# Performance work log

Measured on AMD Instinct MI355X. Metric: run time of the kernel, lower is better.

The kernel has to match this reference:

```python
import jax, jax.numpy as jnp
import numpy as np

N = 50000      # nodes
E = 800000     # edges (before self loops)
G = 64         # graphs in batch
IN = 128       # in_features
HID = 64       # hidden_dim per head
HEADS = 4
NC = 2         # num_classes
SLOPE = 0.2    # PyG GATConv negative_slope default


def setup_inputs() -> dict:
    key = jax.random.key(0)
    ks = jax.random.split(key, 16)
    s = 0.1
    HC = HID * HEADS
    inp = {
        "x": jax.random.normal(ks[0], (N, IN), jnp.float32),
        "edge_index": jax.random.randint(ks[1], (2, E), 0, N, jnp.int64),
        "batch": jnp.sort(jax.random.randint(ks[2], (N,), 0, G, jnp.int64)),
        # GATConv 1: lin weight [H*C, IN], att vecs [H, C], bias [H*C]
        "W1": jax.random.normal(ks[3], (HC, IN), jnp.float32) * s,
        "as1": jax.random.normal(ks[4], (HEADS, HID), jnp.float32) * s,
        "ad1": jax.random.normal(ks[5], (HEADS, HID), jnp.float32) * s,
        "b1": jnp.zeros((HC,), jnp.float32),
        # GATConv 2
        "W2": jax.random.normal(ks[6], (HC, HC), jnp.float32) * s,
        "as2": jax.random.normal(ks[7], (HEADS, HID), jnp.float32) * s,
        "ad2": jax.random.normal(ks[8], (HEADS, HID), jnp.float32) * s,
        "b2": jnp.zeros((HC,), jnp.float32),
        # GATConv 3
        "W3": jax.random.normal(ks[9], (HC, HC), jnp.float32) * s,
        "as3": jax.random.normal(ks[10], (HEADS, HID), jnp.float32) * s,
        "ad3": jax.random.normal(ks[11], (HEADS, HID), jnp.float32) * s,
        "b3": jnp.zeros((HC,), jnp.float32),
        # MLP head
        "fc1_w": jax.random.normal(ks[12], (HID, HC), jnp.float32) * s,
        "fc1_b": jnp.zeros((HID,), jnp.float32),
        "fc2_w": jax.random.normal(ks[13], (NC, HID), jnp.float32) * s,
        "fc2_b": jnp.zeros((NC,), jnp.float32),
    }
    return inp


def gat_conv(x, src, dst, W, a_src, a_dst, b):
    """PyG-style GATConv (concat=True, self loops already in src/dst)."""
    n = x.shape[0]
    h = (x @ W.T).reshape(n, HEADS, HID)            # [N,H,C]
    al_s = jnp.sum(h * a_src[None], axis=-1)        # [N,H]
    al_d = jnp.sum(h * a_dst[None], axis=-1)        # [N,H]
    e = jax.nn.leaky_relu(al_s[src] + al_d[dst], SLOPE)  # [Et,H]
    # segment softmax over edges grouped by destination node
    m = jax.ops.segment_max(e, dst, num_segments=n)      # [N,H]
    ex = jnp.exp(e - m[dst])
    den = jax.ops.segment_sum(ex, dst, num_segments=n)
    alpha = ex / (den[dst] + 1e-16)                      # [Et,H]
    out = jax.ops.segment_sum(h[src] * alpha[:, :, None], dst, num_segments=n)
    return out.reshape(n, HEADS * HID) + b


def reference(x, edge_index, batch, W1, as1, ad1, b1, W2, as2, ad2, b2,
              W3, as3, ad3, b3, fc1_w, fc1_b, fc2_w, fc2_b):
    loops = jnp.arange(N, dtype=edge_index.dtype)
    src = jnp.concatenate([edge_index[0], loops])   # add_self_loops=True
    dst = jnp.concatenate([edge_index[1], loops])

    h = jax.nn.relu(gat_conv(x, src, dst, W1, as1, ad1, b1))
    h = jax.nn.relu(gat_conv(h, src, dst, W2, as2, ad2, b2))
    h = gat_conv(h, src, dst, W3, as3, ad3, b3)

    # global_mean_pool over batch vector
    sums = jax.ops.segment_sum(h, batch, num_segments=G)          # [G,H*C]
    cnts = jax.ops.segment_sum(jnp.ones((N,), h.dtype), batch, num_segments=G)
    pooled = sums / jnp.maximum(cnts, 1.0)[:, None]

    z = jax.nn.relu(pooled @ fc1_w.T + fc1_b)
    return z @ fc2_w.T + fc2_b                                    # [G,NC]
```

## Files before the change

kernel.cpp:

```cpp
#include <hip/hip_runtime.h>
#include <hip/hip_bf16.h>

#define N_NODES 50000
#define E_EDGES 800000
#define ET (E_EDGES + N_NODES)
#define G_GRAPHS 64
#define IN_F 128
#define HID 64
#define HEADS 4
#define HC (HID * HEADS)
#define NC 2
#define SLOPE 0.2f
#define L2E 1.4426950408889634f

typedef float f32x4 __attribute__((ext_vector_type(4)));
typedef __bf16 bf16x8 __attribute__((ext_vector_type(8)));
typedef unsigned short us8 __attribute__((ext_vector_type(8)));
typedef unsigned short us4 __attribute__((ext_vector_type(4)));
typedef _Float16 h16x4 __attribute__((ext_vector_type(4)));

#define MFMA16(a, b, c) \
  __builtin_amdgcn_mfma_f32_16x16x32_bf16(__builtin_bit_cast(bf16x8, (a)), \
                                          __builtin_bit_cast(bf16x8, (b)), (c), 0, 0, 0)

__device__ inline unsigned short f2bf_rne(float f) {
  unsigned u = __builtin_bit_cast(unsigned, f);
  u += 0x7fffu + ((u >> 16) & 1u);
  return (unsigned short)(u >> 16);
}
__device__ inline float bf2f(unsigned short h) {
  unsigned u = ((unsigned)h) << 16;
  return __builtin_bit_cast(float, u);
}


__device__ inline void split4(const float* __restrict__ in, unsigned short* __restrict__ hi,
                              unsigned short* __restrict__ lo, int i) {
  float4 v = *(const float4*)&in[i];
  float f[4] = {v.x, v.y, v.z, v.w};
  us4 h, l;
#pragma unroll
  for (int j = 0; j < 4; j++) {
    unsigned short hb = f2bf_rne(f[j]);
    h[j] = hb;
    l[j] = f2bf_rne(f[j] - bf2f(hb));
  }
  *(us4*)&hi[i] = h;
  *(us4*)&lo[i] = l;
}

#define QX (N_NODES * IN_F / 4)
#define QW1 (HC * IN_F / 4)
#define QW2 (HC * HC / 4)
#define QTOT (QX + QW1 + 2 * QW2)

__global__ __launch_bounds__(256) void split_all_kernel(
    const float* __restrict__ x, const float* __restrict__ W1,
    const float* __restrict__ W2, const float* __restrict__ W3,
    unsigned short* __restrict__ xhi,
    unsigned short* __restrict__ w1h, unsigned short* __restrict__ w1l,
    unsigned short* __restrict__ w2h, unsigned short* __restrict__ w2l,
    unsigned short* __restrict__ w3h, unsigned short* __restrict__ w3l) {
  int q = blockIdx.x * 256 + threadIdx.x;
  if (q < QX) {
    int i = q * 4;
    float4 v = *(const float4*)&x[i];
    float f[4] = {v.x, v.y, v.z, v.w};
    us4 h;
#pragma unroll
    for (int j = 0; j < 4; j++) h[j] = f2bf_rne(f[j]);
    *(us4*)&xhi[i] = h;
  } else if (q < QX + QW1) {
    split4(W1, w1h, w1l, (q - QX) * 4);
  } else if (q < QX + QW1 + QW2) {
    split4(W2, w2h, w2l, (q - QX - QW1) * 4);
  } else {
    split4(W3, w3h, w3l, (q - QX - QW1 - QW2) * 4);
  }
}


__global__ void count_kernel(const int* __restrict__ ei, int* __restrict__ cnt) {
  int e = blockIdx.x * blockDim.x + threadIdx.x;
  if (e >= ET) return;
  int dst = (e < E_EDGES) ? ei[E_EDGES + e] : (e - E_EDGES);
  atomicAdd(&cnt[dst], 1);
}

#define SCAN_BLOCKS ((N_NODES + 255) / 256)

__global__ __launch_bounds__(256) void scan1_kernel(const int* __restrict__ cnt,
                                                    int* __restrict__ incl_buf,
                                                    int* __restrict__ partial) {
  __shared__ int ws[4];
  int tid = threadIdx.x, b = blockIdx.x;
  int wave = tid >> 6, lane = tid & 63;
  int i = b * 256 + tid;
  int v = (i < N_NODES) ? cnt[i] : 0;
  int x = v;
#pragma unroll
  for (int off = 1; off < 64; off <<= 1) {
    int t = __shfl_up(x, off, 64);
    if (lane >= off) x += t;
  }
  if (lane == 63) ws[wave] = x;
  __syncthreads();
  if (tid == 0) {
    int s = 0;
#pragma unroll
    for (int w = 0; w < 4; w++) { int t = ws[w]; ws[w] = s; s += t; }
    partial[b] = s;
  }
  __syncthreads();
  if (i < N_NODES) incl_buf[i] = x + ws[wave];
}

__global__ __launch_bounds__(256) void scan2_kernel(int* __restrict__ partial) {
  __shared__ int ws[4];
  int tid = threadIdx.x;
  int wave = tid >> 6, lane = tid & 63;
  int v = (tid < SCAN_BLOCKS) ? partial[tid] : 0;
  int x = v;
#pragma unroll
  for (int off = 1; off < 64; off <<= 1) {
    int t = __shfl_up(x, off, 64);
    if (lane >= off) x += t;
  }
  if (lane == 63) ws[wave] = x;
  __syncthreads();
  if (tid == 0) {
    int s = 0;
#pragma unroll
    for (int w = 0; w < 4; w++) { int t = ws[w]; ws[w] = s; s += t; }
  }
  __syncthreads();
  partial[tid] = x + ws[wave] - v;
}

__global__ __launch_bounds__(256) void scan3_kernel(const int* __restrict__ cnt,
                                                    int* __restrict__ incl_buf,
                                                    const int* __restrict__ partial,
                                                    int* __restrict__ rowptr,
                                                    int* __restrict__ cursor) {
  int tid = threadIdx.x, b = blockIdx.x;
  int i = b * 256 + tid;
  if (i >= N_NODES) return;
  int incl = incl_buf[i] + partial[b];
  rowptr[i + 1] = incl;
  cursor[i] = incl - cnt[i];
  if (i == 0) rowptr[0] = 0;
}

__global__ void scatter_kernel(const int* __restrict__ ei, int* __restrict__ cursor,
                               int* __restrict__ csr_src) {
  int e = blockIdx.x * blockDim.x + threadIdx.x;
  if (e >= ET) return;
  int src, dst;
  if (e < E_EDGES) { src = ei[e]; dst = ei[E_EDGES + e]; }
  else { src = e - E_EDGES; dst = src; }
  int pos = atomicAdd(&cursor[dst], 1);
  csr_src[pos] = src;
}


template <int K>
__global__ __launch_bounds__(256) void mfma_gemm_kernel(
    const unsigned short* __restrict__ A,
    const unsigned short* __restrict__ Whi, const unsigned short* __restrict__ Wlo,
    const float* __restrict__ a_s, const float* __restrict__ a_d,
    _Float16* __restrict__ hbuf16, float* __restrict__ als, float* __restrict__ ald) {
  __shared__ unsigned short As[4 * 64 * 8];
  __shared__ unsigned short Bs[2][4 * 256 * 8];

  int t = threadIdx.x;
  int mt = blockIdx.x;
  int w = t >> 6, lane = t & 63, lr = lane & 15, kg = lane >> 4;
  int srow = t >> 2, skg = t & 3;

  f32x4 acc[4][4];
#pragma unroll
  for (int m = 0; m < 4; m++)
#pragma unroll
    for (int nf = 0; nf < 4; nf++) {
      f32x4 z = {0.f, 0.f, 0.f, 0.f};
      acc[m][nf] = z;
    }

  int agrow = mt * 64 + srow;
  bool avalid = agrow < N_NODES;

  us8 va[2], vb0[2][4], vb1[2][4];
  {
    if (avalid) {
      va[0] = *(const us8*)&A[(size_t)agrow * K + skg * 8];
    } else {
      us8 z = {0, 0, 0, 0, 0, 0, 0, 0};
      va[0] = z;
    }
#pragma unroll
    for (int c = 0; c < 4; c++) {
      int n = srow + 64 * c;
      vb0[0][c] = *(const us8*)&Whi[(size_t)n * K + skg * 8];
      vb1[0][c] = *(const us8*)&Wlo[(size_t)n * K + skg * 8];
    }
  }

#pragma unroll
  for (int k0 = 0; k0 < K; k0 += 32) {
    const int buf = (k0 >> 5) & 1;
    const int nbuf = buf ^ 1;
    __syncthreads();
    *(us8*)&As[(skg * 64 + srow) * 8] = va[buf];
#pragma unroll
    for (int c = 0; c < 4; c++) {
      int n = srow + 64 * c;
      *(us8*)&Bs[0][(skg * 256 + n) * 8] = vb0[buf][c];
      *(us8*)&Bs[1][(skg * 256 + n) * 8] = vb1[buf][c];
    }
    __syncthreads();

    if (k0 + 32 < K) {
      int k1 = k0 + 32;
      if (avalid) {
        va[nbuf] = *(const us8*)&A[(size_t)agrow * K + k1 + skg * 8];
      } else {
        us8 z = {0, 0, 0, 0, 0, 0, 0, 0};
        va[nbuf] = z;
      }
#pragma unroll
      for (int c = 0; c < 4; c++) {
        int n = srow + 64 * c;
        vb0[nbuf][c] = *(const us8*)&Whi[(size_t)n * K + k1 + skg * 8];
        vb1[nbuf][c] = *(const us8*)&Wlo[(size_t)n * K + k1 + skg * 8];
      }
    }

    us8 bh[4], bl[4];
#pragma unroll
    for (int nf = 0; nf < 4; nf++) {
      int n = w * 64 + nf * 16 + lr;
      bh[nf] = *(us8*)&Bs[0][(kg * 256 + n) * 8];
      bl[nf] = *(us8*)&Bs[1][(kg * 256 + n) * 8];
    }
#pragma unroll
    for (int m = 0; m < 4; m++) {
      int row = m * 16 + lr;
      us8 ah = *(us8*)&As[(kg * 64 + row) * 8];
#pragma unroll
      for (int nf = 0; nf < 4; nf++) {
        acc[m][nf] = MFMA16(ah, bh[nf], acc[m][nf]);
        acc[m][nf] = MFMA16(ah, bl[nf], acc[m][nf]);
      }
    }
  }

  int head = w;
  float asv[4], adv[4];
#pragma unroll
  for (int nf = 0; nf < 4; nf++) {
    asv[nf] = a_s[head * HID + nf * 16 + lr];
    adv[nf] = a_d[head * HID + nf * 16 + lr];
  }
#pragma unroll
  for (int m = 0; m < 4; m++) {
#pragma unroll
    for (int r = 0; r < 4; r++) {
      int grow = mt * 64 + m * 16 + kg * 4 + r;
      float ps = 0.f, pd = 0.f;
#pragma unroll
      for (int nf = 0; nf < 4; nf++) {
        float v = acc[m][nf][r];
        ps += v * asv[nf];
        pd += v * adv[nf];
        if (grow < N_NODES)
          hbuf16[(size_t)grow * HC + head * 64 + nf * 16 + lr] = (_Float16)v;
      }
#pragma unroll
      for (int msk = 1; msk < 16; msk <<= 1) {
        ps += __shfl_xor(ps, msk, 64);
        pd += __shfl_xor(pd, msk, 64);
      }
      if (lr == 0 && grow < N_NODES) {
        als[grow * HEADS + head] = ps * L2E;
        ald[grow * HEADS + head] = pd * L2E;
      }
    }
  }
}


template <int MODE>
__global__ __launch_bounds__(256) void agg_kernel(
    const _Float16* __restrict__ hbuf16, const float* __restrict__ alsE,
    const float* __restrict__ aldE, const int* __restrict__ rowptr,
    const int* __restrict__ csr_src, const float* __restrict__ bias,
    unsigned short* __restrict__ ohi, float* __restrict__ pooled,
    const int* __restrict__ batch) {
  int wave = threadIdx.x >> 6;
  int lane = threadIdx.x & 63;
  int v0 = blockIdx.x * 8 + wave * 2;
  int v1 = v0 + 1;
  int head = lane >> 4;
  float ald0 = aldE[(unsigned)v0 * HEADS + head];
  float ald1 = aldE[(unsigned)v1 * HEADS + head];
  int beg0 = rowptr[v0], n0 = rowptr[v0 + 1] - beg0;
  int beg1 = rowptr[v1], n1 = rowptr[v1 + 1] - beg1;
  int n = max(n0, n1);

  float den0 = 0.f, den1 = 0.f;
  f32x4 acc0 = {0.f, 0.f, 0.f, 0.f};
  f32x4 acc1 = {0.f, 0.f, 0.f, 0.f};
  const _Float16* hp = hbuf16 + (lane << 2);
#pragma unroll 2
  for (int i = 0; i < n; i++) {
    int s0 = csr_src[beg0 + min(i, n0 - 1)];
    int s1 = csr_src[beg1 + min(i, n1 - 1)];
    float a0 = alsE[(unsigned)s0 * HEADS + head] + ald0;
    float a1 = alsE[(unsigned)s1 * HEADS + head] + ald1;
    a0 = fmaxf(a0, SLOPE * a0);
    a1 = fmaxf(a1, SLOPE * a1);
    float ex0 = (i < n0) ? __builtin_amdgcn_exp2f(a0) : 0.f;
    float ex1 = (i < n1) ? __builtin_amdgcn_exp2f(a1) : 0.f;
    h16x4 h0 = *(const h16x4*)(hp + ((unsigned)s0 << 8));
    h16x4 h1 = *(const h16x4*)(hp + ((unsigned)s1 << 8));
    den0 += ex0; den1 += ex1;
    acc0[0] += (float)h0[0] * ex0; acc0[1] += (float)h0[1] * ex0;
    acc0[2] += (float)h0[2] * ex0; acc0[3] += (float)h0[3] * ex0;
    acc1[0] += (float)h1[0] * ex1; acc1[1] += (float)h1[1] * ex1;
    acc1[2] += (float)h1[2] * ex1; acc1[3] += (float)h1[3] * ex1;
  }
  float inv0 = 1.0f / (den0 + 1e-16f);
  float inv1 = 1.0f / (den1 + 1e-16f);
  float4 bv = *(const float4*)&bias[lane * 4];
  float o0[4], o1[4];
  o0[0] = acc0[0] * inv0 + bv.x; o0[1] = acc0[1] * inv0 + bv.y;
  o0[2] = acc0[2] * inv0 + bv.z; o0[3] = acc0[3] * inv0 + bv.w;
  o1[0] = acc1[0] * inv1 + bv.x; o1[1] = acc1[1] * inv1 + bv.y;
  o1[2] = acc1[2] * inv1 + bv.z; o1[3] = acc1[3] * inv1 + bv.w;

  if (MODE == 0) {
    us4 h0, h1;
#pragma unroll
    for (int j = 0; j < 4; j++) {
      h0[j] = f2bf_rne(fmaxf(o0[j], 0.f));
      h1[j] = f2bf_rne(fmaxf(o1[j], 0.f));
    }
    *(us4*)&ohi[(size_t)v0 * HC + lane * 4] = h0;
    *(us4*)&ohi[(size_t)v1 * HC + lane * 4] = h1;
  } else {
    __shared__ float pacc[8][HC];
    __shared__ int pg[8];
    f32x4 ov0 = {o0[0], o0[1], o0[2], o0[3]};
    f32x4 ov1 = {o1[0], o1[1], o1[2], o1[3]};
    *(f32x4*)&pacc[wave * 2][lane * 4] = ov0;
    *(f32x4*)&pacc[wave * 2 + 1][lane * 4] = ov1;
    if (lane == 0) {
      pg[wave * 2] = batch[v0];
      pg[wave * 2 + 1] = batch[v1];
    }
    __syncthreads();
    int c = threadIdx.x;
    float s = pacc[0][c];
    int gcur = pg[0];
#pragma unroll
    for (int wv = 1; wv < 8; wv++) {
      if (pg[wv] != gcur) {
        atomicAdd(&pooled[gcur * HC + c], s);
        s = 0.f;
        gcur = pg[wv];
      }
      s += pacc[wv][c];
    }
    atomicAdd(&pooled[gcur * HC + c], s);
  }
}


__global__ __launch_bounds__(64) void mlp_kernel(const float* __restrict__ pooled_sum,
                                                 const int* __restrict__ batch,
                                                 const float* __restrict__ w1,
                                                 const float* __restrict__ b1,
                                                 const float* __restrict__ w2,
                                                 const float* __restrict__ b2,
                                                 float* __restrict__ out) {
  int g = blockIdx.x;
  int j = threadIdx.x;
  int lo = 0, hi = N_NODES;
  while (lo < hi) { int mid = (lo + hi) >> 1; if (batch[mid] < g) lo = mid + 1; else hi = mid; }
  int start = lo;
  hi = N_NODES;
  while (lo < hi) { int mid = (lo + hi) >> 1; if (batch[mid] < g + 1) lo = mid + 1; else hi = mid; }
  float invc = 1.0f / fmaxf((float)(lo - start), 1.0f);
  __shared__ float z[HID];
  float acc = 0.f;
  for (int k = 0; k < HC; k++) acc += pooled_sum[g * HC + k] * w1[j * HC + k];
  z[j] = fmaxf(acc * invc + b1[j], 0.f);
  __syncthreads();
  if (j < NC) {
    float o = b2[j];
    for (int k = 0; k < HID; k++) o += z[k] * w2[j * HID + k];
    out[g * NC + j] = o;
  }
}


extern "C" void kernel_launch(void* const* d_in, const int* in_sizes, int n_in,
                              void* d_out, int out_size, void* d_ws, size_t ws_size,
                              hipStream_t stream) {
  const float* x    = (const float*)d_in[0];
  const int*   ei   = (const int*)d_in[1];
  const int*   batch= (const int*)d_in[2];
  const float* W1   = (const float*)d_in[3];
  const float* as1  = (const float*)d_in[4];
  const float* ad1  = (const float*)d_in[5];
  const float* b1   = (const float*)d_in[6];
  const float* W2   = (const float*)d_in[7];
  const float* as2  = (const float*)d_in[8];
  const float* ad2  = (const float*)d_in[9];
  const float* b2   = (const float*)d_in[10];
  const float* W3   = (const float*)d_in[11];
  const float* as3  = (const float*)d_in[12];
  const float* ad3  = (const float*)d_in[13];
  const float* b3   = (const float*)d_in[14];
  const float* fc1w = (const float*)d_in[15];
  const float* fc1b = (const float*)d_in[16];
  const float* fc2w = (const float*)d_in[17];
  const float* fc2b = (const float*)d_in[18];
  float* out = (float*)d_out;

  char* ws = (char*)d_ws;
  size_t off = 0;
  _Float16* hbuf16 = (_Float16*)(ws + off); off += (size_t)N_NODES * HC * 2;
  unsigned short* ahi = (unsigned short*)(ws + off); off += (size_t)N_NODES * HC * 2;
  unsigned short* xhi = (unsigned short*)(ws + off); off += (size_t)N_NODES * IN_F * 2;
  unsigned short* w1h = (unsigned short*)(ws + off); off += (size_t)HC * IN_F * 2;
  unsigned short* w1l = (unsigned short*)(ws + off); off += (size_t)HC * IN_F * 2;
  unsigned short* w2h = (unsigned short*)(ws + off); off += (size_t)HC * HC * 2;
  unsigned short* w2l = (unsigned short*)(ws + off); off += (size_t)HC * HC * 2;
  unsigned short* w3h = (unsigned short*)(ws + off); off += (size_t)HC * HC * 2;
  unsigned short* w3l = (unsigned short*)(ws + off); off += (size_t)HC * HC * 2;
  float* als    = (float*)(ws + off); off += (size_t)N_NODES * HEADS * 4;
  float* ald    = (float*)(ws + off); off += (size_t)N_NODES * HEADS * 4;
  float* pooled = (float*)(ws + off); off += (size_t)G_GRAPHS * HC * 4;
  int*   cnt    = (int*)(ws + off);   off += (size_t)N_NODES * 4;
  int*   cursor = (int*)(ws + off);   off += (size_t)N_NODES * 4;
  int*   csrsrc = (int*)(ws + off);   off += (size_t)ET * 4;
  int*   rowptr = (int*)(ws + off);   off += (size_t)(N_NODES + 1) * 4;
  int*   partial= (int*)(ws + off);   off += 256 * 4;

  split_all_kernel<<<(QTOT + 255) / 256, 256, 0, stream>>>(
      x, W1, W2, W3, xhi, w1h, w1l, w2h, w2l, w3h, w3l);

  hipMemsetAsync(cnt, 0, (size_t)N_NODES * 4, stream);
  hipMemsetAsync(pooled, 0, (size_t)G_GRAPHS * HC * 4, stream);
  count_kernel<<<(ET + 255) / 256, 256, 0, stream>>>(ei, cnt);
  scan1_kernel<<<SCAN_BLOCKS, 256, 0, stream>>>(cnt, cursor, partial);
  scan2_kernel<<<1, 256, 0, stream>>>(partial);
  scan3_kernel<<<SCAN_BLOCKS, 256, 0, stream>>>(cnt, cursor, partial, rowptr, cursor);
  scatter_kernel<<<(ET + 255) / 256, 256, 0, stream>>>(ei, cursor, csrsrc);

  dim3 gemm_grid((N_NODES + 63) / 64);
  int agg_grid = N_NODES / 8;

  mfma_gemm_kernel<IN_F><<<gemm_grid, 256, 0, stream>>>(xhi, w1h, w1l, as1, ad1, hbuf16, als, ald);
  agg_kernel<0><<<agg_grid, 256, 0, stream>>>(hbuf16, als, ald, rowptr, csrsrc, b1, ahi, nullptr, nullptr);
  mfma_gemm_kernel<HC><<<gemm_grid, 256, 0, stream>>>(ahi, w2h, w2l, as2, ad2, hbuf16, als, ald);
  agg_kernel<0><<<agg_grid, 256, 0, stream>>>(hbuf16, als, ald, rowptr, csrsrc, b2, ahi, nullptr, nullptr);
  mfma_gemm_kernel<HC><<<gemm_grid, 256, 0, stream>>>(ahi, w3h, w3l, as3, ad3, hbuf16, als, ald);
  agg_kernel<1><<<agg_grid, 256, 0, stream>>>(hbuf16, als, ald, rowptr, csrsrc, b3, nullptr, pooled, batch);

  mlp_kernel<<<G_GRAPHS, 64, 0, stream>>>(pooled, batch, fc1w, fc1b, fc2w, fc2b, out);
}
```

Before: 425.5 us.

## Fold attention vectors into weights and compute attention logits via extra MFMA

Precomputes W^T·a_src and W^T·a_dst (scaled by log2 e) as split bf16 hi/lo matrices in the prep kernel. Each GEMM now produces the per-node attention logits through two extra MFMAs per row tile, replacing the dot-product and 16-lane shuffle reduction in the epilogue. Node buffers are padded so the GEMM can drop its row bounds checks. In exchange, every wave issues more MFMAs, all four waves compute the logit tile redundantly, and the padded rows read uninitialized workspace data that is then discarded.

```diff
diff --git a/kernel.cpp b/kernel.cpp
--- a/kernel.cpp
+++ b/kernel.cpp
@@ -2,6 +2,7 @@
 #include <hip/hip_bf16.h>
 
 #define N_NODES 50000
+#define NPAD (N_NODES + 64)
 #define E_EDGES 800000
 #define ET (E_EDGES + N_NODES)
 #define G_GRAPHS 64
@@ -53,14 +54,22 @@
 #define QW1 (HC * IN_F / 4)
 #define QW2 (HC * HC / 4)
 #define QTOT (QX + QW1 + 2 * QW2)
+#define QWALS (8 * IN_F + 8 * HC + 8 * HC)
+#define QALL (QTOT + QWALS)
 
 __global__ __launch_bounds__(256) void split_all_kernel(
     const float* __restrict__ x, const float* __restrict__ W1,
     const float* __restrict__ W2, const float* __restrict__ W3,
+    const float* __restrict__ as1, const float* __restrict__ ad1,
+    const float* __restrict__ as2, const float* __restrict__ ad2,
+    const float* __restrict__ as3, const float* __restrict__ ad3,
     unsigned short* __restrict__ xhi,
     unsigned short* __restrict__ w1h, unsigned short* __restrict__ w1l,
     unsigned short* __restrict__ w2h, unsigned short* __restrict__ w2l,
-    unsigned short* __restrict__ w3h, unsigned short* __restrict__ w3l) {
+    unsigned short* __restrict__ w3h, unsigned short* __restrict__ w3l,
+    unsigned short* __restrict__ wa1h, unsigned short* __restrict__ wa1l,
+    unsigned short* __restrict__ wa2h, unsigned short* __restrict__ wa2l,
+    unsigned short* __restrict__ wa3h, unsigned short* __restrict__ wa3l) {
   int q = blockIdx.x * 256 + threadIdx.x;
   if (q < QX) {
     int i = q * 4;
@@ -74,8 +83,33 @@
     split4(W1, w1h, w1l, (q - QX) * 4);
   } else if (q < QX + QW1 + QW2) {
     split4(W2, w2h, w2l, (q - QX - QW1) * 4);
-  } else {
+  } else if (q < QTOT) {
     split4(W3, w3h, w3l, (q - QX - QW1 - QW2) * 4);
+  } else if (q < QALL) {
+    int q2 = q - QTOT;
+    const float *W, *av;
+    unsigned short *wh, *wl;
+    int j, k, K;
+    if (q2 < 8 * IN_F) {
+      j = q2 >> 7; k = q2 & (IN_F - 1); K = IN_F;
+      W = W1; av = (j < 4) ? as1 : ad1; wh = wa1h; wl = wa1l;
+    } else if (q2 < 8 * IN_F + 8 * HC) {
+      int r = q2 - 8 * IN_F;
+      j = r >> 8; k = r & (HC - 1); K = HC;
+      W = W2; av = (j < 4) ? as2 : ad2; wh = wa2h; wl = wa2l;
+    } else {
+      int r = q2 - 8 * IN_F - 8 * HC;
+      j = r >> 8; k = r & (HC - 1); K = HC;
+      W = W3; av = (j < 4) ? as3 : ad3; wh = wa3h; wl = wa3l;
+    }
+    int head = j & 3;
+    float s = 0.f;
+    for (int c = 0; c < HID; c++)
+      s += av[head * HID + c] * W[(size_t)(head * HID + c) * K + k];
+    s *= L2E;
+    unsigned short hb = f2bf_rne(s);
+    wh[j * K + k] = hb;
+    wl[j * K + k] = f2bf_rne(s - bf2f(hb));
   }
 }
 
@@ -167,7 +201,7 @@
 __global__ __launch_bounds__(256) void mfma_gemm_kernel(
     const unsigned short* __restrict__ A,
     const unsigned short* __restrict__ Whi, const unsigned short* __restrict__ Wlo,
-    const float* __restrict__ a_s, const float* __restrict__ a_d,
+    const unsigned short* __restrict__ Walsh, const unsigned short* __restrict__ Walsl,
     _Float16* __restrict__ hbuf16, float* __restrict__ als, float* __restrict__ ald) {
   __shared__ unsigned short As[4 * 64 * 8];
   __shared__ unsigned short Bs[2][4 * 256 * 8];
@@ -178,32 +212,30 @@
   int srow = t >> 2, skg = t & 3;
 
   f32x4 acc[4][4];
-#pragma unroll
-  for (int m = 0; m < 4; m++)
+  f32x4 accal[4];
+#pragma unroll
+  for (int m = 0; m < 4; m++) {
 #pragma unroll
     for (int nf = 0; nf < 4; nf++) {
       f32x4 z = {0.f, 0.f, 0.f, 0.f};
       acc[m][nf] = z;
     }
+    f32x4 z = {0.f, 0.f, 0.f, 0.f};
+    accal[m] = z;
+  }
 
   int agrow = mt * 64 + srow;
-  bool avalid = agrow < N_NODES;
-
-  us8 va[2], vb0[2][4], vb1[2][4];
-  {
-    if (avalid) {
-      va[0] = *(const us8*)&A[(size_t)agrow * K + skg * 8];
-    } else {
-      us8 z = {0, 0, 0, 0, 0, 0, 0, 0};
-      va[0] = z;
-    }
-#pragma unroll
-    for (int c = 0; c < 4; c++) {
-      int n = srow + 64 * c;
-      vb0[0][c] = *(const us8*)&Whi[(size_t)n * K + skg * 8];
-      vb1[0][c] = *(const us8*)&Wlo[(size_t)n * K + skg * 8];
-    }
-  }
+
+  us8 va[2], vb0[2][4], vb1[2][4], wh[2], wl[2];
+  va[0] = *(const us8*)&A[(size_t)agrow * K + skg * 8];
+#pragma unroll
+  for (int c = 0; c < 4; c++) {
+    int n = srow + 64 * c;
+    vb0[0][c] = *(const us8*)&Whi[(size_t)n * K + skg * 8];
+    vb1[0][c] = *(const us8*)&Wlo[(size_t)n * K + skg * 8];
+  }
+  wh[0] = *(const us8*)&Walsh[lr * K + kg * 8];
+  wl[0] = *(const us8*)&Walsl[lr * K + kg * 8];
 
 #pragma unroll
   for (int k0 = 0; k0 < K; k0 += 32) {
@@ -221,18 +253,15 @@
 
     if (k0 + 32 < K) {
       int k1 = k0 + 32;
-      if (avalid) {
-        va[nbuf] = *(const us8*)&A[(size_t)agrow * K + k1 + skg * 8];
-      } else {
-        us8 z = {0, 0, 0, 0, 0, 0, 0, 0};
-        va[nbuf] = z;
-      }
+      va[nbuf] = *(const us8*)&A[(size_t)agrow * K + k1 + skg * 8];
 #pragma unroll
       for (int c = 0; c < 4; c++) {
         int n = srow + 64 * c;
         vb0[nbuf][c] = *(const us8*)&Whi[(size_t)n * K + k1 + skg * 8];
         vb1[nbuf][c] = *(const us8*)&Wlo[(size_t)n * K + k1 + skg * 8];
       }
+      wh[nbuf] = *(const us8*)&Walsh[lr * K + k1 + kg * 8];
+      wl[nbuf] = *(const us8*)&Walsl[lr * K + k1 + kg * 8];
     }
 
     us8 bh[4], bl[4];
@@ -251,38 +280,30 @@
         acc[m][nf] = MFMA16(ah, bh[nf], acc[m][nf]);
         acc[m][nf] = MFMA16(ah, bl[nf], acc[m][nf]);
       }
+      accal[m] = MFMA16(ah, wh[buf], accal[m]);
+      accal[m] = MFMA16(ah, wl[buf], accal[m]);
     }
   }
 
   int head = w;
-  float asv[4], adv[4];
-#pragma unroll
-  for (int nf = 0; nf < 4; nf++) {
-    asv[nf] = a_s[head * HID + nf * 16 + lr];
-    adv[nf] = a_d[head * HID + nf * 16 + lr];
-  }
 #pragma unroll
   for (int m = 0; m < 4; m++) {
 #pragma unroll
     for (int r = 0; r < 4; r++) {
       int grow = mt * 64 + m * 16 + kg * 4 + r;
-      float ps = 0.f, pd = 0.f;
-#pragma unroll
-      for (int nf = 0; nf < 4; nf++) {
-        float v = acc[m][nf][r];
-        ps += v * asv[nf];
-        pd += v * adv[nf];
-        if (grow < N_NODES)
-          hbuf16[(size_t)grow * HC + head * 64 + nf * 16 + lr] = (_Float16)v;
-      }
-#pragma unroll
-      for (int msk = 1; msk < 16; msk <<= 1) {
-        ps += __shfl_xor(ps, msk, 64);
-        pd += __shfl_xor(pd, msk, 64);
-      }
-      if (lr == 0 && grow < N_NODES) {
-        als[grow * HEADS + head] = ps * L2E;
-        ald[grow * HEADS + head] = pd * L2E;
+#pragma unroll
+      for (int nf = 0; nf < 4; nf++)
+        hbuf16[(size_t)grow * HC + head * 64 + nf * 16 + lr] = (_Float16)acc[m][nf][r];
+    }
+  }
+  if (w == 0) {
+#pragma unroll
+    for (int m = 0; m < 4; m++) {
+#pragma unroll
+      for (int r = 0; r < 4; r++) {
+        int grow = mt * 64 + m * 16 + kg * 4 + r;
+        if (lr < 4) als[grow * HEADS + lr] = accal[m][r];
+        else if (lr < 8) ald[grow * HEADS + (lr - 4)] = accal[m][r];
       }
     }
   }
@@ -430,17 +451,23 @@
 
   char* ws = (char*)d_ws;
   size_t off = 0;
-  _Float16* hbuf16 = (_Float16*)(ws + off); off += (size_t)N_NODES * HC * 2;
-  unsigned short* ahi = (unsigned short*)(ws + off); off += (size_t)N_NODES * HC * 2;
-  unsigned short* xhi = (unsigned short*)(ws + off); off += (size_t)N_NODES * IN_F * 2;
+  _Float16* hbuf16 = (_Float16*)(ws + off); off += (size_t)NPAD * HC * 2;
+  unsigned short* ahi = (unsigned short*)(ws + off); off += (size_t)NPAD * HC * 2;
+  unsigned short* xhi = (unsigned short*)(ws + off); off += (size_t)NPAD * IN_F * 2;
   unsigned short* w1h = (unsigned short*)(ws + off); off += (size_t)HC * IN_F * 2;
   unsigned short* w1l = (unsigned short*)(ws + off); off += (size_t)HC * IN_F * 2;
   unsigned short* w2h = (unsigned short*)(ws + off); off += (size_t)HC * HC * 2;
   unsigned short* w2l = (unsigned short*)(ws + off); off += (size_t)HC * HC * 2;
   unsigned short* w3h = (unsigned short*)(ws + off); off += (size_t)HC * HC * 2;
   unsigned short* w3l = (unsigned short*)(ws + off); off += (size_t)HC * HC * 2;
-  float* als    = (float*)(ws + off); off += (size_t)N_NODES * HEADS * 4;
-  float* ald    = (float*)(ws + off); off += (size_t)N_NODES * HEADS * 4;
+  unsigned short* wa1h = (unsigned short*)(ws + off); off += (size_t)16 * IN_F * 2;
+  unsigned short* wa1l = (unsigned short*)(ws + off); off += (size_t)16 * IN_F * 2;
+  unsigned short* wa2h = (unsigned short*)(ws + off); off += (size_t)16 * HC * 2;
+  unsigned short* wa2l = (unsigned short*)(ws + off); off += (size_t)16 * HC * 2;
+  unsigned short* wa3h = (unsigned short*)(ws + off); off += (size_t)16 * HC * 2;
+  unsigned short* wa3l = (unsigned short*)(ws + off); off += (size_t)16 * HC * 2;
+  float* als    = (float*)(ws + off); off += (size_t)NPAD * HEADS * 4;
+  float* ald    = (float*)(ws + off); off += (size_t)NPAD * HEADS * 4;
   float* pooled = (float*)(ws + off); off += (size_t)G_GRAPHS * HC * 4;
   int*   cnt    = (int*)(ws + off);   off += (size_t)N_NODES * 4;
   int*   cursor = (int*)(ws + off);   off += (size_t)N_NODES * 4;
@@ -448,8 +475,10 @@
   int*   rowptr = (int*)(ws + off);   off += (size_t)(N_NODES + 1) * 4;
   int*   partial= (int*)(ws + off);   off += 256 * 4;
 
-  split_all_kernel<<<(QTOT + 255) / 256, 256, 0, stream>>>(
-      x, W1, W2, W3, xhi, w1h, w1l, w2h, w2l, w3h, w3l);
+  split_all_kernel<<<(QALL + 255) / 256, 256, 0, stream>>>(
+      x, W1, W2, W3, as1, ad1, as2, ad2, as3, ad3,
+      xhi, w1h, w1l, w2h, w2l, w3h, w3l,
+      wa1h, wa1l, wa2h, wa2l, wa3h, wa3l);
 
   hipMemsetAsync(cnt, 0, (size_t)N_NODES * 4, stream);
   hipMemsetAsync(pooled, 0, (size_t)G_GRAPHS * HC * 4, stream);
@@ -462,11 +491,11 @@
   dim3 gemm_grid((N_NODES + 63) / 64);
   int agg_grid = N_NODES / 8;
 
-  mfma_gemm_kernel<IN_F><<<gemm_grid, 256, 0, stream>>>(xhi, w1h, w1l, as1, ad1, hbuf16, als, ald);
+  mfma_gemm_kernel<IN_F><<<gemm_grid, 256, 0, stream>>>(xhi, w1h, w1l, wa1h, wa1l, hbuf16, als, ald);
   agg_kernel<0><<<agg_grid, 256, 0, stream>>>(hbuf16, als, ald, rowptr, csrsrc, b1, ahi, nullptr, nullptr);
-  mfma_gemm_kernel<HC><<<gemm_grid, 256, 0, stream>>>(ahi, w2h, w2l, as2, ad2, hbuf16, als, ald);
+  mfma_gemm_kernel<HC><<<gemm_grid, 256, 0, stream>>>(ahi, w2h, w2l, wa2h, wa2l, hbuf16, als, ald);
   agg_kernel<0><<<agg_grid, 256, 0, stream>>>(hbuf16, als, ald, rowptr, csrsrc, b2, ahi, nullptr, nullptr);
-  mfma_gemm_kernel<HC><<<gemm_grid, 256, 0, stream>>>(ahi, w3h, w3l, as3, ad3, hbuf16, als, ald);
+  mfma_gemm_kernel<HC><<<gemm_grid, 256, 0, stream>>>(ahi, w3h, w3l, wa3h, wa3l, hbuf16, als, ald);
   agg_kernel<1><<<agg_grid, 256, 0, stream>>>(hbuf16, als, ald, rowptr, csrsrc, b3, nullptr, pooled, batch);
 
   mlp_kernel<<<G_GRAPHS, 64, 0, stream>>>(pooled, batch, fc1w, fc1b, fc2w, fc2b, out);
```

After: 446.7 us. 5.0% more time.
